# Performance work log

Hardware: AMD Instinct MI355X
Metric: run time of the kernel (lower is better)

## Reference

```python
import jax, jax.numpy as jnp
import numpy as np

B, H, W, C = 4, 64, 64, 256
CP = C // 2  # downsize_factor = 2

def setup_inputs() -> dict:
    key = jax.random.key(0)
    ks = jax.random.split(key, 5)
    s = 1.0 / np.sqrt(C)
    return {
        "x": jax.random.normal(ks[0], (B, H, W, C), dtype=jnp.float32),
        "Wk": jax.random.normal(ks[1], (C, CP), dtype=jnp.float32) * s,
        "bk": jnp.zeros((CP,), dtype=jnp.float32),
        "Wq": jax.random.normal(ks[2], (C, CP), dtype=jnp.float32) * s,
        "bq": jnp.zeros((CP,), dtype=jnp.float32),
        "Wv": jax.random.normal(ks[3], (C, CP), dtype=jnp.float32) * s,
        "bv": jnp.zeros((CP,), dtype=jnp.float32),
        "Ws": jax.random.normal(ks[4], (C, CP), dtype=jnp.float32) * s,
        "bs": jnp.zeros((CP,), dtype=jnp.float32),
    }

def reference(x, Wk, bk, Wq, bq, Wv, bv, Ws, bs):
    b, h, w, c = x.shape
    n = h * w
    xf = x.reshape(b, n, c)  # 1x1 conv == per-pixel matmul
    K = xf @ Wk + bk  # [b, n, c']
    Q = xf @ Wq + bq  # [b, n, c']
    V = xf @ Wv + bv  # [b, n, c']
    # Keras Dot(axes=(2,1))([K, Q^T]) -> scores = K @ Q^T (no 1/sqrt(d) scaling)
    scores = jnp.einsum('bnc,bmc->bnm', K, Q)
    attn = jax.nn.softmax(scores, axis=-1)
    out = jnp.einsum('bnm,bmc->bnc', attn, V)  # [b, n, c']
    shortcut = xf @ Ws + bs  # downsize_factor > 1 path
    return (out + shortcut).reshape(b, h, w, out.shape[-1])
```

## Files before the change

kernel.cpp:

```cpp
#include <hip/hip_runtime.h>
#include <math.h>

typedef unsigned short u16;
typedef __attribute__((ext_vector_type(8))) _Float16 half8;
typedef __attribute__((ext_vector_type(4))) float    f32x4;

#define BATCH 4
#define NPB   4096
#define BN    16384
#define CC    256
#define D     128
#define LOG2E 1.44269504088896f

#if __has_builtin(__builtin_amdgcn_exp2f)
#define EXP2(x) __builtin_amdgcn_exp2f(x)
#else
#define EXP2(x) exp2f(x)
#endif

template<int CTRL>
__device__ __forceinline__ float dpp_mov(float x) {
    return __builtin_bit_cast(float, __builtin_amdgcn_update_dpp(
        __builtin_bit_cast(int, x), __builtin_bit_cast(int, x),
        CTRL, 0xf, 0xf, false));
}
__device__ __forceinline__ float dpp_row_max(float x) {
    x = fmaxf(x, dpp_mov<0x128>(x));
    x = fmaxf(x, dpp_mov<0x124>(x));
    x = fmaxf(x, dpp_mov<0x122>(x));
    x = fmaxf(x, dpp_mov<0x121>(x));
    return x;
}
__device__ __forceinline__ float dpp_row_sum(float x) {
    x += dpp_mov<0x128>(x);
    x += dpp_mov<0x124>(x);
    x += dpp_mov<0x122>(x);
    x += dpp_mov<0x121>(x);
    return x;
}

__global__ __launch_bounds__(256) void prep_kernel(
    const float* __restrict__ Wk, const float* __restrict__ Wq,
    const float* __restrict__ Wv, const float* __restrict__ Ws,
    u16* __restrict__ Wt)
{
    const int f   = (blockIdx.x * 256 + threadIdx.x) * 4;
    const int mat = f >> 15;
    const int rem = f & 32767;
    const int c   = rem >> 8;
    const int k0  = rem & 255;
    const float* W = (mat == 0) ? Wk : (mat == 1) ? Wq : (mat == 2) ? Wv : Ws;
    const float scale = (mat == 0) ? LOG2E : 1.0f;
    _Float16 t4[4];
#pragma unroll
    for (int i = 0; i < 4; ++i)
        t4[i] = (_Float16)(W[(size_t)(k0 + i) * D + c] * scale);
    *(uint2*)&Wt[(size_t)mat * 32768 + (size_t)c * 256 + k0] = *(const uint2*)t4;
}

#define APJ 264

__global__ __launch_bounds__(256, 2) void proj_kernel(
    const float* __restrict__ x, const u16* __restrict__ Wt,
    const float* __restrict__ bk, const float* __restrict__ bq,
    const float* __restrict__ bv, const float* __restrict__ bs,
    u16* __restrict__ Kh, u16* __restrict__ Qf,
    u16* __restrict__ Vf, float* __restrict__ Sc)
{
    __shared__ __align__(16) u16 As[128][APJ];

    const int tid = threadIdx.x;
    const int wv  = tid >> 6;
    const int l   = tid & 63;
    const int l15 = l & 15;
    const int l4  = l >> 4;
    const int by  = blockIdx.y;
    const int gm0 = blockIdx.x * 128;
    const int c0  = wv * 32;

    const u16* wb = Wt + (size_t)by * 32768 + (size_t)(c0 + l15) * 256 + l4 * 8;
    half8 wf[2][8];
#pragma unroll
    for (int ct = 0; ct < 2; ++ct)
#pragma unroll
        for (int kc = 0; kc < 8; ++kc)
            wf[ct][kc] = *(const half8*)(wb + ct * 16 * 256 + kc * 32);

    {
        const float4* xg = (const float4*)(x + (size_t)gm0 * CC);
#pragma unroll 8
        for (int i = 0; i < 32; ++i) {
            const int f = i * 256 + tid;
            const float4 v = xg[f];
            const int row = f >> 6, col4 = f & 63;
            _Float16 h[4] = {(_Float16)v.x, (_Float16)v.y,
                             (_Float16)v.z, (_Float16)v.w};
            *(uint2*)&As[row][col4 * 4] = *(const uint2*)h;
        }
    }
    __syncthreads();

    f32x4 acc[8][2];
#pragma unroll
    for (int mt = 0; mt < 8; ++mt) {
        acc[mt][0] = (f32x4){0.f, 0.f, 0.f, 0.f};
        acc[mt][1] = (f32x4){0.f, 0.f, 0.f, 0.f};
    }

    if (by == 2) {
        for (int kc = 0; kc < 8; ++kc)
#pragma unroll
            for (int mt = 0; mt < 8; ++mt) {
                const half8 a = *(const half8*)&As[mt * 16 + l15][kc * 32 + l4 * 8];
                acc[mt][0] = __builtin_amdgcn_mfma_f32_16x16x32_f16(a, wf[0][kc], acc[mt][0], 0, 0, 0);
                acc[mt][1] = __builtin_amdgcn_mfma_f32_16x16x32_f16(a, wf[1][kc], acc[mt][1], 0, 0, 0);
            }
        const float bb[2] = {bv[c0 + l15], bv[c0 + 16 + l15]};
        const int batch = gm0 >> 12;
        const int mb    = (gm0 & 4095) >> 5;
        u16* vbp = Vf + (size_t)batch * (D * NPB);
#pragma unroll
        for (int mt = 0; mt < 8; ++mt)
#pragma unroll
            for (int ct = 0; ct < 2; ++ct) {
                _Float16 t4[4];
#pragma unroll
                for (int r = 0; r < 4; ++r)
                    t4[r] = (_Float16)(acc[mt][ct][r] + bb[ct]);
                const int blk = (mb + (mt >> 1)) * 8 + wv * 2 + ct;
                const int off = blk * 512 + l15 * 32 + (mt & 1) * 16 + l4 * 4;
                *(uint2*)&vbp[off] = *(const uint2*)t4;
            }
    } else {
        for (int kc = 0; kc < 8; ++kc)
#pragma unroll
            for (int mt = 0; mt < 8; ++mt) {
                const half8 a = *(const half8*)&As[mt * 16 + l15][kc * 32 + l4 * 8];
                acc[mt][0] = __builtin_amdgcn_mfma_f32_16x16x32_f16(wf[0][kc], a, acc[mt][0], 0, 0, 0);
                acc[mt][1] = __builtin_amdgcn_mfma_f32_16x16x32_f16(wf[1][kc], a, acc[mt][1], 0, 0, 0);
            }
        if (by == 3) {
            float bb2[2][4];
#pragma unroll
            for (int ct = 0; ct < 2; ++ct)
#pragma unroll
                for (int r = 0; r < 4; ++r)
                    bb2[ct][r] = bs[c0 + ct * 16 + l4 * 4 + r];
#pragma unroll
            for (int mt = 0; mt < 8; ++mt) {
                const int m = gm0 + mt * 16 + l15;
#pragma unroll
                for (int ct = 0; ct < 2; ++ct) {
                    float4 v;
                    v.x = acc[mt][ct][0] + bb2[ct][0];
                    v.y = acc[mt][ct][1] + bb2[ct][1];
                    v.z = acc[mt][ct][2] + bb2[ct][2];
                    v.w = acc[mt][ct][3] + bb2[ct][3];
                    *(float4*)&Sc[(size_t)m * D + c0 + ct * 16 + l4 * 4] = v;
                }
            }
        } else if (by == 1) {
            float bb2[2][4];
#pragma unroll
            for (int ct = 0; ct < 2; ++ct)
#pragma unroll
                for (int r = 0; r < 4; ++r)
                    bb2[ct][r] = bq[c0 + ct * 16 + l4 * 4 + r];
#pragma unroll
            for (int mt = 0; mt < 8; ++mt) {
                const int blk = (((gm0 >> 4) + mt) << 2) + wv;
#pragma unroll
                for (int ct = 0; ct < 2; ++ct) {
                    _Float16 t4[4];
#pragma unroll
                    for (int r = 0; r < 4; ++r)
                        t4[r] = (_Float16)(acc[mt][ct][r] + bb2[ct][r]);
                    const int off = blk * 512 + (ct * 2 + (l4 >> 1)) * 128
                                    + l15 * 8 + (l4 & 1) * 4;
                    *(uint2*)&Qf[off] = *(const uint2*)t4;
                }
            }
        } else {
            float bb2[2][4];
#pragma unroll
            for (int ct = 0; ct < 2; ++ct)
#pragma unroll
                for (int r = 0; r < 4; ++r)
                    bb2[ct][r] = bk[c0 + ct * 16 + l4 * 4 + r] * LOG2E;
#pragma unroll
            for (int mt = 0; mt < 8; ++mt) {
                const int m = gm0 + mt * 16 + l15;
#pragma unroll
                for (int ct = 0; ct < 2; ++ct) {
                    _Float16 t4[4];
#pragma unroll
                    for (int r = 0; r < 4; ++r)
                        t4[r] = (_Float16)(acc[mt][ct][r] + bb2[ct][r]);
                    *(uint2*)&Kh[(size_t)m * D + c0 + ct * 16 + l4 * 4] =
                        *(const uint2*)t4;
                }
            }
        }
    }
}

#define VPP 40
#define OBP 132

__global__ __launch_bounds__(256, 2) void attn_kernel(
    const u16* __restrict__ Kh, const u16* __restrict__ Qf,
    const u16* __restrict__ Vf, const float* __restrict__ Sc,
    float* __restrict__ out)
{
    __shared__ __align__(16) u16   Ps[4][2][16][VPP];
    __shared__ __align__(16) float Obuf[4][32][OBP];
    __shared__ float ml[4][2][32];

    const int tid = threadIdx.x;
    const int wv  = tid >> 6;
    const int l   = tid & 63;
    const int l15 = l & 15;
    const int l4  = l >> 4;

    const int bx    = blockIdx.x;
    const int xcd   = bx & 7;
    const int batch = xcd >> 1;
    const int tile  = ((xcd & 1) << 6) | (bx >> 3);
    const int gr0   = batch * NPB + tile * 32;

    half8 kf[2][4];
#pragma unroll
    for (int nt = 0; nt < 2; ++nt)
#pragma unroll
        for (int kc = 0; kc < 4; ++kc)
            kf[nt][kc] = *(const half8*)(
                Kh + (size_t)(gr0 + nt * 16 + l15) * D + kc * 32 + l4 * 8);

    const int  qtb = (batch * NPB + wv * 1024) >> 4;
    const int  vbb = wv * 32;
    const u16* vb  = Vf + (size_t)batch * (D * NPB);
    const int  vl  = l15 * 4 + l4;

    f32x4 Oc[2][8];
#pragma unroll
    for (int nt = 0; nt < 2; ++nt)
#pragma unroll
        for (int ct = 0; ct < 8; ++ct)
            Oc[nt][ct] = (f32x4){0.f, 0.f, 0.f, 0.f};
    float mold[2][4], lsum[2][4];
#pragma unroll
    for (int nt = 0; nt < 2; ++nt)
#pragma unroll
        for (int r = 0; r < 4; ++r) { mold[nt][r] = -1e30f; lsum[nt][r] = 0.f; }

    for (int it = 0; it < 32; ++it) {
        half8 qf[2][4];
#pragma unroll
        for (int mt = 0; mt < 2; ++mt)
#pragma unroll
            for (int kc = 0; kc < 4; ++kc)
                qf[mt][kc] = *(const half8*)(
                    Qf + (size_t)(((qtb + it * 2 + mt) << 2) + kc) * 512 + l * 8);
        half8 vf[8];
#pragma unroll
        for (int ct = 0; ct < 8; ++ct)
            vf[ct] = *(const half8*)(
                vb + (size_t)(((vbb + it) << 3) + ct) * 512 + vl * 8);

        f32x4 sacc[2][2];
        sacc[0][0] = (f32x4){0.f, 0.f, 0.f, 0.f};
        sacc[0][1] = (f32x4){0.f, 0.f, 0.f, 0.f};
        sacc[1][0] = (f32x4){0.f, 0.f, 0.f, 0.f};
        sacc[1][1] = (f32x4){0.f, 0.f, 0.f, 0.f};
        __builtin_amdgcn_s_setprio(1);
#pragma unroll
        for (int kc = 0; kc < 4; ++kc)
#pragma unroll
            for (int nt = 0; nt < 2; ++nt)
#pragma unroll
                for (int mt = 0; mt < 2; ++mt)
                    sacc[nt][mt] = __builtin_amdgcn_mfma_f32_16x16x32_f16(
                        kf[nt][kc], qf[mt][kc], sacc[nt][mt], 0, 0, 0);
        __builtin_amdgcn_s_setprio(0);

#pragma unroll
        for (int nt = 0; nt < 2; ++nt)
#pragma unroll
            for (int r = 0; r < 4; ++r) {
                const float rmax  = dpp_row_max(fmaxf(sacc[nt][0][r], sacc[nt][1][r]));
                const float mnew  = fmaxf(mold[nt][r], rmax);
                const float alpha = EXP2(mold[nt][r] - mnew);
                mold[nt][r] = mnew;
                const float p0 = EXP2(sacc[nt][0][r] - mnew);
                const float p1 = EXP2(sacc[nt][1][r] - mnew);
                lsum[nt][r] = lsum[nt][r] * alpha + p0 + p1;
#pragma unroll
                for (int ct = 0; ct < 8; ++ct) Oc[nt][ct][r] *= alpha;
                Ps[wv][nt][l4 * 4 + r][l15]      = __builtin_bit_cast(u16, (_Float16)p0);
                Ps[wv][nt][l4 * 4 + r][16 + l15] = __builtin_bit_cast(u16, (_Float16)p1);
            }
        asm volatile("s_waitcnt lgkmcnt(0)" ::: "memory");

        __builtin_amdgcn_s_setprio(1);
#pragma unroll
        for (int nt = 0; nt < 2; ++nt) {
            const half8 pf = *(const half8*)&Ps[wv][nt][l15][l4 * 8];
#pragma unroll
            for (int ct = 0; ct < 8; ++ct)
                Oc[nt][ct] = __builtin_amdgcn_mfma_f32_16x16x32_f16(
                    pf, vf[ct], Oc[nt][ct], 0, 0, 0);
        }
        __builtin_amdgcn_s_setprio(0);
    }

#pragma unroll
    for (int nt = 0; nt < 2; ++nt)
#pragma unroll
        for (int r = 0; r < 4; ++r)
            lsum[nt][r] = dpp_row_sum(lsum[nt][r]);

    if (l15 == 0) {
#pragma unroll
        for (int nt = 0; nt < 2; ++nt)
#pragma unroll
            for (int r = 0; r < 4; ++r) {
                ml[wv][0][nt * 16 + l4 * 4 + r] = mold[nt][r];
                ml[wv][1][nt * 16 + l4 * 4 + r] = lsum[nt][r];
            }
    }
    __syncthreads();

#pragma unroll
    for (int nt = 0; nt < 2; ++nt)
#pragma unroll
        for (int r = 0; r < 4; ++r) {
            const int row = nt * 16 + l4 * 4 + r;
            const float M = fmaxf(fmaxf(ml[0][0][row], ml[1][0][row]),
                                  fmaxf(ml[2][0][row], ml[3][0][row]));
            const float fw = EXP2(mold[nt][r] - M);
#pragma unroll
            for (int ct = 0; ct < 8; ++ct)
                Obuf[wv][row][ct * 16 + l15] = Oc[nt][ct][r] * fw;
        }
    __syncthreads();

    {
        const int row = wv * 8 + (l >> 3);
        const int cb  = (l & 7) * 16;
        const float M = fmaxf(fmaxf(ml[0][0][row], ml[1][0][row]),
                              fmaxf(ml[2][0][row], ml[3][0][row]));
        float L = 0.f;
#pragma unroll
        for (int s = 0; s < 4; ++s)
            L += ml[s][1][row] * EXP2(ml[s][0][row] - M);
        const float invL = 1.f / L;
        const size_t grow = (size_t)(gr0 + row);
#pragma unroll
        for (int j = 0; j < 4; ++j) {
            const int c = cb + j * 4;
            f32x4 a = *(const f32x4*)&Obuf[0][row][c];
#pragma unroll
            for (int s = 1; s < 4; ++s) {
                const f32x4 b2 = *(const f32x4*)&Obuf[s][row][c];
                a[0] += b2[0]; a[1] += b2[1]; a[2] += b2[2]; a[3] += b2[3];
            }
            const float4 sc = *(const float4*)&Sc[grow * D + c];
            float4 o;
            o.x = a[0] * invL + sc.x;
            o.y = a[1] * invL + sc.y;
            o.z = a[2] * invL + sc.z;
            o.w = a[3] * invL + sc.w;
            *(float4*)&out[grow * D + c] = o;
        }
    }
}

extern "C" void kernel_launch(void* const* d_in, const int* in_sizes, int n_in,
                              void* d_out, int out_size, void* d_ws, size_t ws_size,
                              hipStream_t stream) {
    const float* x  = (const float*)d_in[0];
    const float* Wk = (const float*)d_in[1];
    const float* bk = (const float*)d_in[2];
    const float* Wq = (const float*)d_in[3];
    const float* bq = (const float*)d_in[4];
    const float* Wv = (const float*)d_in[5];
    const float* bv = (const float*)d_in[6];
    const float* Ws = (const float*)d_in[7];
    const float* bs = (const float*)d_in[8];
    float* out = (float*)d_out;

    u16*   Kh = (u16*)d_ws;
    u16*   Qf = Kh + (size_t)BN * D;
    u16*   Vf = Qf + (size_t)BN * D;
    float* Sc = (float*)(Vf + (size_t)BN * D);
    u16*   Wt = (u16*)(Sc + (size_t)BN * D);

    prep_kernel<<<128, 256, 0, stream>>>(Wk, Wq, Wv, Ws, Wt);
    proj_kernel<<<dim3(128, 4), 256, 0, stream>>>(x, Wt, bk, bq, bv, bs,
                                                  Kh, Qf, Vf, Sc);
    attn_kernel<<<512, 256, 0, stream>>>(Kh, Qf, Vf, Sc, out);
}
```

Baseline: 151.0 us.

## Add lazy softmax rescaling and halve epilogue LDS buffer for higher occupancy

The online softmax now rescales the output accumulators and running sum only when some row's max grows by more than a threshold (THR=8 in log2 units). This skips the per-tile alpha exp and the 64 multiplies in the common case. The cross-wave combine buffer shrinks from four slices to two: waves 2-3 write their slices, then waves 0-1 accumulate into them. That cuts LDS use so launch bounds can request 3 blocks per CU. The lazy rescale allows unnormalized P values up to 2^8, which risks fp16 precision or overflow, and the added barrier and divergent branch add some overhead.

Measured after the change: 212.6 us. 1.41x slower.

```diff
diff --git a/kernel.cpp b/kernel.cpp
--- a/kernel.cpp
+++ b/kernel.cpp
@@ -11,6 +11,7 @@
 #define CC    256
 #define D     128
 #define LOG2E 1.44269504088896f
+#define THR   8.0f
 
 #if __has_builtin(__builtin_amdgcn_exp2f)
 #define EXP2(x) __builtin_amdgcn_exp2f(x)
@@ -207,13 +208,13 @@
 #define VPP 40
 #define OBP 132
 
-__global__ __launch_bounds__(256, 2) void attn_kernel(
+__global__ __launch_bounds__(256, 3) void attn_kernel(
     const u16* __restrict__ Kh, const u16* __restrict__ Qf,
     const u16* __restrict__ Vf, const float* __restrict__ Sc,
     float* __restrict__ out)
 {
     __shared__ __align__(16) u16   Ps[4][2][16][VPP];
-    __shared__ __align__(16) float Obuf[4][32][OBP];
+    __shared__ __align__(16) float Obuf[2][32][OBP];
     __shared__ float ml[4][2][32];
 
     const int tid = threadIdx.x;
@@ -283,19 +284,35 @@
                         kf[nt][kc], qf[mt][kc], sacc[nt][mt], 0, 0, 0);
         __builtin_amdgcn_s_setprio(0);
 
+        float rmax[2][4];
+        int grow = 0;
 #pragma unroll
         for (int nt = 0; nt < 2; ++nt)
 #pragma unroll
             for (int r = 0; r < 4; ++r) {
-                const float rmax  = dpp_row_max(fmaxf(sacc[nt][0][r], sacc[nt][1][r]));
-                const float mnew  = fmaxf(mold[nt][r], rmax);
-                const float alpha = EXP2(mold[nt][r] - mnew);
-                mold[nt][r] = mnew;
-                const float p0 = EXP2(sacc[nt][0][r] - mnew);
-                const float p1 = EXP2(sacc[nt][1][r] - mnew);
-                lsum[nt][r] = lsum[nt][r] * alpha + p0 + p1;
-#pragma unroll
-                for (int ct = 0; ct < 8; ++ct) Oc[nt][ct][r] *= alpha;
+                rmax[nt][r] = dpp_row_max(fmaxf(sacc[nt][0][r], sacc[nt][1][r]));
+                grow |= (rmax[nt][r] > mold[nt][r] + THR) ? 1 : 0;
+            }
+        if (__any(grow)) {
+#pragma unroll
+            for (int nt = 0; nt < 2; ++nt)
+#pragma unroll
+                for (int r = 0; r < 4; ++r) {
+                    const float mnew  = fmaxf(mold[nt][r], rmax[nt][r]);
+                    const float alpha = EXP2(mold[nt][r] - mnew);
+                    mold[nt][r] = mnew;
+                    lsum[nt][r] *= alpha;
+#pragma unroll
+                    for (int ct = 0; ct < 8; ++ct) Oc[nt][ct][r] *= alpha;
+                }
+        }
+#pragma unroll
+        for (int nt = 0; nt < 2; ++nt)
+#pragma unroll
+            for (int r = 0; r < 4; ++r) {
+                const float p0 = EXP2(sacc[nt][0][r] - mold[nt][r]);
+                const float p1 = EXP2(sacc[nt][1][r] - mold[nt][r]);
+                lsum[nt][r] += p0 + p1;
                 Ps[wv][nt][l4 * 4 + r][l15]      = __builtin_bit_cast(u16, (_Float16)p0);
                 Ps[wv][nt][l4 * 4 + r][16 + l15] = __builtin_bit_cast(u16, (_Float16)p1);
             }
@@ -330,6 +347,7 @@
     }
     __syncthreads();
 
+    float fw[2][4];
 #pragma unroll
     for (int nt = 0; nt < 2; ++nt)
 #pragma unroll
@@ -337,11 +355,32 @@
             const int row = nt * 16 + l4 * 4 + r;
             const float M = fmaxf(fmaxf(ml[0][0][row], ml[1][0][row]),
                                   fmaxf(ml[2][0][row], ml[3][0][row]));
-            const float fw = EXP2(mold[nt][r] - M);
-#pragma unroll
-            for (int ct = 0; ct < 8; ++ct)
-                Obuf[wv][row][ct * 16 + l15] = Oc[nt][ct][r] * fw;
-        }
+            fw[nt][r] = EXP2(mold[nt][r] - M);
+        }
+
+    if (wv >= 2) {
+#pragma unroll
+        for (int nt = 0; nt < 2; ++nt)
+#pragma unroll
+            for (int r = 0; r < 4; ++r) {
+                const int row = nt * 16 + l4 * 4 + r;
+#pragma unroll
+                for (int ct = 0; ct < 8; ++ct)
+                    Obuf[wv - 2][row][ct * 16 + l15] = Oc[nt][ct][r] * fw[nt][r];
+            }
+    }
+    __syncthreads();
+    if (wv < 2) {
+#pragma unroll
+        for (int nt = 0; nt < 2; ++nt)
+#pragma unroll
+            for (int r = 0; r < 4; ++r) {
+                const int row = nt * 16 + l4 * 4 + r;
+#pragma unroll
+                for (int ct = 0; ct < 8; ++ct)
+                    Obuf[wv][row][ct * 16 + l15] += Oc[nt][ct][r] * fw[nt][r];
+            }
+    }
     __syncthreads();
 
     {
@@ -354,23 +393,19 @@
         for (int s = 0; s < 4; ++s)
             L += ml[s][1][row] * EXP2(ml[s][0][row] - M);
         const float invL = 1.f / L;
-        const size_t grow = (size_t)(gr0 + row);
+        const size_t grow_ = (size_t)(gr0 + row);
 #pragma unroll
         for (int j = 0; j < 4; ++j) {
             const int c = cb + j * 4;
-            f32x4 a = *(const f32x4*)&Obuf[0][row][c];
-#pragma unroll
-            for (int s = 1; s < 4; ++s) {
-                const f32x4 b2 = *(const f32x4*)&Obuf[s][row][c];
-                a[0] += b2[0]; a[1] += b2[1]; a[2] += b2[2]; a[3] += b2[3];
-            }
-            const float4 sc = *(const float4*)&Sc[grow * D + c];
+            const f32x4 a = *(const f32x4*)&Obuf[0][row][c];
+            const f32x4 b = *(const f32x4*)&Obuf[1][row][c];
+            const float4 sc = *(const float4*)&Sc[grow_ * D + c];
             float4 o;
-            o.x = a[0] * invL + sc.x;
-            o.y = a[1] * invL + sc.y;
-            o.z = a[2] * invL + sc.z;
-            o.w = a[3] * invL + sc.w;
-            *(float4*)&out[grow * D + c] = o;
+            o.x = (a[0] + b[0]) * invL + sc.x;
+            o.y = (a[1] + b[1]) * invL + sc.y;
+            o.z = (a[2] + b[2]) * invL + sc.z;
+            o.w = (a[3] + b[3]) * invL + sc.w;
+            *(float4*)&out[grow_ * D + c] = o;
         }
     }
 }
```

## Pre-convert x to fp16 MFMA-fragment layout and drop LDS staging in projection

Applied to the files above, without the earlier changes.

The prep kernel now also converts x to fp16 and writes it in a blocked layout that matches the MFMA A/B fragment order. The projection kernel then loads fragments straight from global memory into registers, with no shared-memory tile and no block barrier, and accumulates one 16-row tile at a time. This removes the LDS traffic and the sync, and shrinks register use for accumulators. In exchange it adds an extra global write and read of the fp16 x (about 8 MB), and each of the 4 projection groups rereads x from global or L2.

After: 157.7 us. +4.4%, slower.

```diff
diff --git a/kernel.cpp b/kernel.cpp
--- a/kernel.cpp
+++ b/kernel.cpp
@@ -42,33 +42,45 @@
 __global__ __launch_bounds__(256) void prep_kernel(
     const float* __restrict__ Wk, const float* __restrict__ Wq,
     const float* __restrict__ Wv, const float* __restrict__ Ws,
-    u16* __restrict__ Wt)
+    const float* __restrict__ x,
+    u16* __restrict__ Wt, u16* __restrict__ xf)
 {
-    const int f   = (blockIdx.x * 256 + threadIdx.x) * 4;
-    const int mat = f >> 15;
-    const int rem = f & 32767;
-    const int c   = rem >> 8;
-    const int k0  = rem & 255;
-    const float* W = (mat == 0) ? Wk : (mat == 1) ? Wq : (mat == 2) ? Wv : Ws;
-    const float scale = (mat == 0) ? LOG2E : 1.0f;
-    _Float16 t4[4];
-#pragma unroll
-    for (int i = 0; i < 4; ++i)
-        t4[i] = (_Float16)(W[(size_t)(k0 + i) * D + c] * scale);
-    *(uint2*)&Wt[(size_t)mat * 32768 + (size_t)c * 256 + k0] = *(const uint2*)t4;
-}
-
-#define APJ 264
+    const int bx = blockIdx.x;
+    if (bx < 128) {
+        const int f   = (bx * 256 + threadIdx.x) * 4;
+        const int mat = f >> 15;
+        const int rem = f & 32767;
+        const int c   = rem >> 8;
+        const int k0  = rem & 255;
+        const float* W = (mat == 0) ? Wk : (mat == 1) ? Wq : (mat == 2) ? Wv : Ws;
+        const float scale = (mat == 0) ? LOG2E : 1.0f;
+        _Float16 t4[4];
+#pragma unroll
+        for (int i = 0; i < 4; ++i)
+            t4[i] = (_Float16)(W[(size_t)(k0 + i) * D + c] * scale);
+        *(uint2*)&Wt[(size_t)mat * 32768 + (size_t)c * 256 + k0] = *(const uint2*)t4;
+    } else {
+        const int g   = (bx - 128) * 256 + threadIdx.x;
+        const int f   = g * 8;
+        const int blk = f >> 9;
+        const int o   = (f >> 3) & 63;
+        const int m   = (blk >> 3) * 16 + (o & 15);
+        const int k   = (blk & 7) * 32 + (o >> 4) * 8;
+        const float4* xs = (const float4*)(x + (size_t)m * CC + k);
+        const float4 a = xs[0], b = xs[1];
+        _Float16 h[8] = {(_Float16)a.x, (_Float16)a.y, (_Float16)a.z, (_Float16)a.w,
+                         (_Float16)b.x, (_Float16)b.y, (_Float16)b.z, (_Float16)b.w};
+        *(uint4*)&xf[f] = *(const uint4*)h;
+    }
+}
 
 __global__ __launch_bounds__(256, 2) void proj_kernel(
-    const float* __restrict__ x, const u16* __restrict__ Wt,
+    const u16* __restrict__ xf, const u16* __restrict__ Wt,
     const float* __restrict__ bk, const float* __restrict__ bq,
     const float* __restrict__ bv, const float* __restrict__ bs,
     u16* __restrict__ Kh, u16* __restrict__ Qf,
     u16* __restrict__ Vf, float* __restrict__ Sc)
 {
-    __shared__ __align__(16) u16 As[128][APJ];
-
     const int tid = threadIdx.x;
     const int wv  = tid >> 6;
     const int l   = tid & 63;
@@ -86,119 +98,133 @@
         for (int kc = 0; kc < 8; ++kc)
             wf[ct][kc] = *(const half8*)(wb + ct * 16 * 256 + kc * 32);
 
-    {
-        const float4* xg = (const float4*)(x + (size_t)gm0 * CC);
-#pragma unroll 8
-        for (int i = 0; i < 32; ++i) {
-            const int f = i * 256 + tid;
-            const float4 v = xg[f];
-            const int row = f >> 6, col4 = f & 63;
-            _Float16 h[4] = {(_Float16)v.x, (_Float16)v.y,
-                             (_Float16)v.z, (_Float16)v.w};
-            *(uint2*)&As[row][col4 * 4] = *(const uint2*)h;
-        }
-    }
-    __syncthreads();
-
-    f32x4 acc[8][2];
-#pragma unroll
-    for (int mt = 0; mt < 8; ++mt) {
-        acc[mt][0] = (f32x4){0.f, 0.f, 0.f, 0.f};
-        acc[mt][1] = (f32x4){0.f, 0.f, 0.f, 0.f};
-    }
+    const u16* xb = xf + ((size_t)(gm0 >> 4) * 8) * 512 + l * 8;
 
     if (by == 2) {
-        for (int kc = 0; kc < 8; ++kc)
-#pragma unroll
-            for (int mt = 0; mt < 8; ++mt) {
-                const half8 a = *(const half8*)&As[mt * 16 + l15][kc * 32 + l4 * 8];
-                acc[mt][0] = __builtin_amdgcn_mfma_f32_16x16x32_f16(a, wf[0][kc], acc[mt][0], 0, 0, 0);
-                acc[mt][1] = __builtin_amdgcn_mfma_f32_16x16x32_f16(a, wf[1][kc], acc[mt][1], 0, 0, 0);
-            }
         const float bb[2] = {bv[c0 + l15], bv[c0 + 16 + l15]};
         const int batch = gm0 >> 12;
         const int mb    = (gm0 & 4095) >> 5;
         u16* vbp = Vf + (size_t)batch * (D * NPB);
 #pragma unroll
-        for (int mt = 0; mt < 8; ++mt)
+        for (int mt = 0; mt < 8; ++mt) {
+            half8 xv[8];
+#pragma unroll
+            for (int kc = 0; kc < 8; ++kc)
+                xv[kc] = *(const half8*)(xb + (mt * 8 + kc) * 512);
+            f32x4 acc[2];
+            acc[0] = (f32x4){0.f, 0.f, 0.f, 0.f};
+            acc[1] = (f32x4){0.f, 0.f, 0.f, 0.f};
+#pragma unroll
+            for (int kc = 0; kc < 8; ++kc) {
+                acc[0] = __builtin_amdgcn_mfma_f32_16x16x32_f16(xv[kc], wf[0][kc], acc[0], 0, 0, 0);
+                acc[1] = __builtin_amdgcn_mfma_f32_16x16x32_f16(xv[kc], wf[1][kc], acc[1], 0, 0, 0);
+            }
 #pragma unroll
             for (int ct = 0; ct < 2; ++ct) {
                 _Float16 t4[4];
 #pragma unroll
                 for (int r = 0; r < 4; ++r)
-                    t4[r] = (_Float16)(acc[mt][ct][r] + bb[ct]);
+                    t4[r] = (_Float16)(acc[ct][r] + bb[ct]);
                 const int blk = (mb + (mt >> 1)) * 8 + wv * 2 + ct;
                 const int off = blk * 512 + l15 * 32 + (mt & 1) * 16 + l4 * 4;
                 *(uint2*)&vbp[off] = *(const uint2*)t4;
             }
+        }
+    } else if (by == 3) {
+        float bb2[2][4];
+#pragma unroll
+        for (int ct = 0; ct < 2; ++ct)
+#pragma unroll
+            for (int r = 0; r < 4; ++r)
+                bb2[ct][r] = bs[c0 + ct * 16 + l4 * 4 + r];
+#pragma unroll
+        for (int mt = 0; mt < 8; ++mt) {
+            half8 xv[8];
+#pragma unroll
+            for (int kc = 0; kc < 8; ++kc)
+                xv[kc] = *(const half8*)(xb + (mt * 8 + kc) * 512);
+            f32x4 acc[2];
+            acc[0] = (f32x4){0.f, 0.f, 0.f, 0.f};
+            acc[1] = (f32x4){0.f, 0.f, 0.f, 0.f};
+#pragma unroll
+            for (int kc = 0; kc < 8; ++kc) {
+                acc[0] = __builtin_amdgcn_mfma_f32_16x16x32_f16(wf[0][kc], xv[kc], acc[0], 0, 0, 0);
+                acc[1] = __builtin_amdgcn_mfma_f32_16x16x32_f16(wf[1][kc], xv[kc], acc[1], 0, 0, 0);
+            }
+            const int m = gm0 + mt * 16 + l15;
+#pragma unroll
+            for (int ct = 0; ct < 2; ++ct) {
+                float4 v;
+                v.x = acc[ct][0] + bb2[ct][0];
+                v.y = acc[ct][1] + bb2[ct][1];
+                v.z = acc[ct][2] + bb2[ct][2];
+                v.w = acc[ct][3] + bb2[ct][3];
+                *(float4*)&Sc[(size_t)m * D + c0 + ct * 16 + l4 * 4] = v;
+            }
+        }
+    } else if (by == 1) {
+        float bb2[2][4];
+#pragma unroll
+        for (int ct = 0; ct < 2; ++ct)
+#pragma unroll
+            for (int r = 0; r < 4; ++r)
+                bb2[ct][r] = bq[c0 + ct * 16 + l4 * 4 + r];
+#pragma unroll
+        for (int mt = 0; mt < 8; ++mt) {
+            half8 xv[8];
+#pragma unroll
+            for (int kc = 0; kc < 8; ++kc)
+                xv[kc] = *(const half8*)(xb + (mt * 8 + kc) * 512);
+            f32x4 acc[2];
+            acc[0] = (f32x4){0.f, 0.f, 0.f, 0.f};
+            acc[1] = (f32x4){0.f, 0.f, 0.f, 0.f};
+#pragma unroll
+            for (int kc = 0; kc < 8; ++kc) {
+                acc[0] = __builtin_amdgcn_mfma_f32_16x16x32_f16(wf[0][kc], xv[kc], acc[0], 0, 0, 0);
+                acc[1] = __builtin_amdgcn_mfma_f32_16x16x32_f16(wf[1][kc], xv[kc], acc[1], 0, 0, 0);
+            }
+            const int blk = (((gm0 >> 4) + mt) << 2) + wv;
+#pragma unroll
+            for (int ct = 0; ct < 2; ++ct) {
+                _Float16 t4[4];
+#pragma unroll
+                for (int r = 0; r < 4; ++r)
+                    t4[r] = (_Float16)(acc[ct][r] + bb2[ct][r]);
+                const int off = blk * 512 + (ct * 2 + (l4 >> 1)) * 128
+                                + l15 * 8 + (l4 & 1) * 4;
+                *(uint2*)&Qf[off] = *(const uint2*)t4;
+            }
+        }
     } else {
-        for (int kc = 0; kc < 8; ++kc)
-#pragma unroll
-            for (int mt = 0; mt < 8; ++mt) {
-                const half8 a = *(const half8*)&As[mt * 16 + l15][kc * 32 + l4 * 8];
-                acc[mt][0] = __builtin_amdgcn_mfma_f32_16x16x32_f16(wf[0][kc], a, acc[mt][0], 0, 0, 0);
-                acc[mt][1] = __builtin_amdgcn_mfma_f32_16x16x32_f16(wf[1][kc], a, acc[mt][1], 0, 0, 0);
-            }
-        if (by == 3) {
-            float bb2[2][4];
-#pragma unroll
-            for (int ct = 0; ct < 2; ++ct)
+        float bb2[2][4];
+#pragma unroll
+        for (int ct = 0; ct < 2; ++ct)
+#pragma unroll
+            for (int r = 0; r < 4; ++r)
+                bb2[ct][r] = bk[c0 + ct * 16 + l4 * 4 + r] * LOG2E;
+#pragma unroll
+        for (int mt = 0; mt < 8; ++mt) {
+            half8 xv[8];
+#pragma unroll
+            for (int kc = 0; kc < 8; ++kc)
+                xv[kc] = *(const half8*)(xb + (mt * 8 + kc) * 512);
+            f32x4 acc[2];
+            acc[0] = (f32x4){0.f, 0.f, 0.f, 0.f};
+            acc[1] = (f32x4){0.f, 0.f, 0.f, 0.f};
+#pragma unroll
+            for (int kc = 0; kc < 8; ++kc) {
+                acc[0] = __builtin_amdgcn_mfma_f32_16x16x32_f16(wf[0][kc], xv[kc], acc[0], 0, 0, 0);
+                acc[1] = __builtin_amdgcn_mfma_f32_16x16x32_f16(wf[1][kc], xv[kc], acc[1], 0, 0, 0);
+            }
+            const int m = gm0 + mt * 16 + l15;
+#pragma unroll
+            for (int ct = 0; ct < 2; ++ct) {
+                _Float16 t4[4];
 #pragma unroll
                 for (int r = 0; r < 4; ++r)
-                    bb2[ct][r] = bs[c0 + ct * 16 + l4 * 4 + r];
-#pragma unroll
-            for (int mt = 0; mt < 8; ++mt) {
-                const int m = gm0 + mt * 16 + l15;
-#pragma unroll
-                for (int ct = 0; ct < 2; ++ct) {
-                    float4 v;
-                    v.x = acc[mt][ct][0] + bb2[ct][0];
-                    v.y = acc[mt][ct][1] + bb2[ct][1];
-                    v.z = acc[mt][ct][2] + bb2[ct][2];
-                    v.w = acc[mt][ct][3] + bb2[ct][3];
-                    *(float4*)&Sc[(size_t)m * D + c0 + ct * 16 + l4 * 4] = v;
-                }
-            }
-        } else if (by == 1) {
-            float bb2[2][4];
-#pragma unroll
-            for (int ct = 0; ct < 2; ++ct)
-#pragma unroll
-                for (int r = 0; r < 4; ++r)
-                    bb2[ct][r] = bq[c0 + ct * 16 + l4 * 4 + r];
-#pragma unroll
-            for (int mt = 0; mt < 8; ++mt) {
-                const int blk = (((gm0 >> 4) + mt) << 2) + wv;
-#pragma unroll
-                for (int ct = 0; ct < 2; ++ct) {
-                    _Float16 t4[4];
-#pragma unroll
-                    for (int r = 0; r < 4; ++r)
-                        t4[r] = (_Float16)(acc[mt][ct][r] + bb2[ct][r]);
-                    const int off = blk * 512 + (ct * 2 + (l4 >> 1)) * 128
-                                    + l15 * 8 + (l4 & 1) * 4;
-                    *(uint2*)&Qf[off] = *(const uint2*)t4;
-                }
-            }
-        } else {
-            float bb2[2][4];
-#pragma unroll
-            for (int ct = 0; ct < 2; ++ct)
-#pragma unroll
-                for (int r = 0; r < 4; ++r)
-                    bb2[ct][r] = bk[c0 + ct * 16 + l4 * 4 + r] * LOG2E;
-#pragma unroll
-            for (int mt = 0; mt < 8; ++mt) {
-                const int m = gm0 + mt * 16 + l15;
-#pragma unroll
-                for (int ct = 0; ct < 2; ++ct) {
-                    _Float16 t4[4];
-#pragma unroll
-                    for (int r = 0; r < 4; ++r)
-                        t4[r] = (_Float16)(acc[mt][ct][r] + bb2[ct][r]);
-                    *(uint2*)&Kh[(size_t)m * D + c0 + ct * 16 + l4 * 4] =
-                        *(const uint2*)t4;
-                }
+                    t4[r] = (_Float16)(acc[ct][r] + bb2[ct][r]);
+                *(uint2*)&Kh[(size_t)m * D + c0 + ct * 16 + l4 * 4] =
+                    *(const uint2*)t4;
             }
         }
     }
@@ -394,9 +420,10 @@
     u16*   Vf = Qf + (size_t)BN * D;
     float* Sc = (float*)(Vf + (size_t)BN * D);
     u16*   Wt = (u16*)(Sc + (size_t)BN * D);
-
-    prep_kernel<<<128, 256, 0, stream>>>(Wk, Wq, Wv, Ws, Wt);
-    proj_kernel<<<dim3(128, 4), 256, 0, stream>>>(x, Wt, bk, bq, bv, bs,
+    u16*   xf = Wt + 4 * 32768;
+
+    prep_kernel<<<128 + 2048, 256, 0, stream>>>(Wk, Wq, Wv, Ws, x, Wt, xf);
+    proj_kernel<<<dim3(128, 4), 256, 0, stream>>>(xf, Wt, bk, bq, bv, bs,
                                                   Kh, Qf, Vf, Sc);
     attn_kernel<<<512, 256, 0, stream>>>(Kh, Qf, Vf, Sc, out);
 }
```
